# Kernel tuning notes

Measured on AMD Instinct MI355X. Metric: run time of the kernel, lower is better.

Reference implementation:

```python
import jax, jax.numpy as jnp
import numpy as np

N_NEAR = 16
BN_EPS = 1e-5


def fps(xyz, n_center):
    # farthest point sampling, deterministic start at index 0. xyz: [B,N,C]
    B, N, _ = xyz.shape
    dist0 = jnp.full((B, N), jnp.inf, dtype=xyz.dtype)
    far0 = jnp.zeros((B,), dtype=jnp.int32)

    def step(carry, _):
        dist, far = carry
        centroid = jnp.take_along_axis(xyz, far[:, None, None], axis=1)  # [B,1,C]
        d = jnp.sum((xyz - centroid) ** 2, axis=-1)                       # [B,N]
        dist = jnp.minimum(dist, d)
        nxt = jnp.argmax(dist, axis=-1).astype(jnp.int32)
        return (dist, nxt), far

    _, idxs = jax.lax.scan(step, (dist0, far0), None, length=n_center)
    return jnp.transpose(idxs)  # [B, n_center]


def knn(xyz, k):
    # k nearest neighbors (self included), xyz: [B,N,C] -> idx [B,N,k]
    sq = jnp.sum(xyz * xyz, axis=-1)
    d = sq[:, :, None] - 2.0 * jnp.einsum('bnc,bmc->bnm', xyz, xyz) + sq[:, None, :]
    _, idx = jax.lax.top_k(-d, k)
    return idx


def gather_points(x, idx):
    # x: [B,N,...], idx: [B,*dims] int -> [B,*dims,...]
    return jax.vmap(lambda xb, ib: xb[ib])(x, idx)


def conv_bn_relu(x, W, b, g, be):
    # x: [B,C,K,S]; 1x1 Conv2d + BatchNorm2d (training/batch stats) + ReLU
    y = jnp.einsum('oc,bcks->boks', W, x) + b[None, :, None, None]
    mean = jnp.mean(y, axis=(0, 2, 3), keepdims=True)
    var = jnp.mean((y - mean) ** 2, axis=(0, 2, 3), keepdims=True)  # biased var, as torch BN
    y = (y - mean) * jax.lax.rsqrt(var + BN_EPS)
    y = y * g[None, :, None, None] + be[None, :, None, None]
    return jax.nn.relu(y)


def setup_inputs() -> dict:
    key = jax.random.key(0)
    ks = jax.random.split(key, 8)
    B, N, EMB = 16, 2048, 64
    mlp = [64, 128, 256]
    in_ch = 2 + EMB
    inp = {
        'xy': jax.random.normal(ks[0], (B, 2, N), dtype=jnp.float32),
        'fea': jax.random.normal(ks[1], (B, EMB, N), dtype=jnp.float32),
    }
    last = in_ch
    for i, out in enumerate(mlp):
        inp[f'W{i+1}'] = 0.1 * jax.random.normal(ks[2 + i], (out, last), dtype=jnp.float32)
        inp[f'b{i+1}'] = jnp.zeros((out,), dtype=jnp.float32)
        inp[f'g{i+1}'] = jnp.ones((out,), dtype=jnp.float32)
        inp[f'be{i+1}'] = jnp.zeros((out,), dtype=jnp.float32)
        last = out
    return inp


def reference(xy, fea, W1, b1, g1, be1, W2, b2, g2, be2, W3, b3, g3, be3):
    B, _, N = xy.shape
    n_center = N // 2 + 1
    xyz = jnp.transpose(xy, (0, 2, 1))   # [B,N,2]
    f = jnp.transpose(fea, (0, 2, 1))    # [B,N,emb]

    fps_idx = fps(xyz, n_center)                      # [B,S]
    new_xyz = gather_points(xyz, fps_idx)             # [B,S,2]
    knn_idx = knn(xyz, N_NEAR)                        # [B,N,k]
    knn_of_fps = gather_points(knn_idx, fps_idx)      # [B,S,k]
    grouped_xyz = gather_points(xyz, knn_of_fps)      # [B,S,k,2]
    grouped_norm = grouped_xyz - new_xyz[:, :, None, :]
    grouped_f = gather_points(f, knn_of_fps)          # [B,S,k,emb]
    new_fea = jnp.concatenate([grouped_norm, grouped_f], axis=-1)  # [B,S,k,C]

    x = jnp.transpose(new_fea, (0, 3, 2, 1))          # [B,C,k,S]
    for (W, b, g, be) in ((W1, b1, g1, be1), (W2, b2, g2, be2), (W3, b3, g3, be3)):
        x = conv_bn_relu(x, W, b, g, be)
    out = jnp.max(x, axis=2)                          # [B,C_out,S]
    return jnp.transpose(new_xyz, (0, 2, 1)), out
```

## Files before the change

kernel.cpp:

```cpp
#include <hip/hip_runtime.h>
#include <math.h>

#define B_   16
#define N_   2048
#define S_   1025
#define K_   16
#define EMB_ 64
#define NF_  (B_ * S_ * K_)
#define NCH_ (NF_ / 64)
#define NBS_ (NCH_ * 4)
#define NBLK 256
#define PK_UNITS 513
#define KNN_ITEMS (129 * 16)

typedef float v2f __attribute__((ext_vector_type(2)));
typedef short bf16x8 __attribute__((ext_vector_type(8)));
typedef float f32x4 __attribute__((ext_vector_type(4)));

#define AL(p)    __hip_atomic_load((p), __ATOMIC_ACQUIRE, __HIP_MEMORY_SCOPE_AGENT)
#define ALR(p)   __hip_atomic_load((p), __ATOMIC_RELAXED, __HIP_MEMORY_SCOPE_AGENT)
#define ASR(p,v) __hip_atomic_store((p), (v), __ATOMIC_RELEASE, __HIP_MEMORY_SCOPE_AGENT)
#define AADD(p)  __hip_atomic_fetch_add((p), 1, __ATOMIC_ACQ_REL, __HIP_MEMORY_SCOPE_AGENT)

__device__ __forceinline__ unsigned short f2bf(float f) {
  unsigned u = __float_as_uint(f);
  u += 0x7fffu + ((u >> 16) & 1u);
  return (unsigned short)(u >> 16);
}
__device__ __forceinline__ float bfl(unsigned pk) { return __uint_as_float((pk & 0xffffu) << 16); }
__device__ __forceinline__ float bfh(unsigned pk) { return __uint_as_float(pk & 0xffff0000u); }

__device__ __forceinline__ float rowsum16(float v) {
#define RADD(CTRL) { int tm_ = __builtin_amdgcn_update_dpp(0, __float_as_int(v), (CTRL), 0xF, 0xF, true); \
                     v += __int_as_float(tm_); }
  RADD(0x111) RADD(0x112) RADD(0x114) RADD(0x118)
#undef RADD
  return v;
}

__global__ void diag_kernel(float* out, float v) {
  if (threadIdx.x == 0 && blockIdx.x == 0) out[0] = v;
}

__global__ __launch_bounds__(256, 1)
void phase0_kernel(const float* __restrict__ xy, const float* __restrict__ fea,
                   const float* __restrict__ W1,
                   const float* __restrict__ W2, const float* __restrict__ W3,
                   int* fps_idx, float* new_xyz, int* knn_sel,
                   unsigned* Pp, unsigned short* W2b, unsigned short* W3b,
                   float* out0, int* flags) {
  __shared__ float2 sh_lxy[N_];
  __shared__ double sh_lsq[N_];
  __shared__ float sh_pkA[4096];
  __shared__ float sh_pkB[4096];
  __shared__ int sh_unit;
  const int bid = blockIdx.x;
  const int tid = threadIdx.x;
  int* progress = flags + 8;

  if (bid < 16) {
    const int b = bid;
    const int lane = tid;
    const float* xb = xy + (size_t)b * 2 * N_;
    v2f pxp[16], pyp[16];
    float dist[32];
    if (lane < 64) {
      const float2* xb2 = (const float2*)xb;
      const float2* yb2 = (const float2*)(xb + N_);
#pragma unroll
      for (int q = 0; q < 16; ++q) {
        float2 x01 = xb2[lane * 16 + q];
        float2 y01 = yb2[lane * 16 + q];
        int p = lane * 32 + 2 * q;
        sh_lxy[p] = make_float2(x01.x, y01.x);
        sh_lxy[p + 1] = make_float2(x01.y, y01.y);
        pxp[q][0] = x01.x; pxp[q][1] = x01.y;
        pyp[q][0] = y01.x; pyp[q][1] = y01.y;
        dist[2 * q] = __builtin_inff();
        dist[2 * q + 1] = __builtin_inff();
      }
#pragma unroll
      for (int q = 0; q < 16; ++q) {
        asm volatile("" : "+v"(pxp[q]), "+v"(pyp[q]));
      }
    }
    __syncthreads();
    if (lane < 64) {
      int cur = 0;
      for (int t = 0; t < S_; ++t) {
        float2 c = sh_lxy[cur];
        if (lane == 0) {
          fps_idx[b * S_ + t] = cur;
          new_xyz[(b * S_ + t) * 2 + 0] = c.x;
          new_xyz[(b * S_ + t) * 2 + 1] = c.y;
          out0[b * 2 * S_ + t] = c.x;
          out0[b * 2 * S_ + S_ + t] = c.y;
        }
        const float ncx = -c.x, ncy = -c.y;
        v2f ncx2; ncx2[0] = ncx; ncx2[1] = ncx;
        v2f ncy2; ncy2[0] = ncy; ncy2[1] = ncy;
#pragma unroll
        for (int q = 0; q < 16; ++q) {
          v2f dx, dy, sx, sy, dd;
          asm("v_pk_add_f32 %0, %1, %2" : "=v"(dx) : "v"(pxp[q]), "v"(ncx2));
          asm("v_pk_add_f32 %0, %1, %2" : "=v"(dy) : "v"(pyp[q]), "v"(ncy2));
          asm("v_pk_mul_f32 %0, %1, %1" : "=v"(sx) : "v"(dx));
          asm("v_pk_mul_f32 %0, %1, %1" : "=v"(sy) : "v"(dy));
          asm("v_pk_add_f32 %0, %1, %2" : "=v"(dd) : "v"(sx), "v"(sy));
          dist[2 * q] = fminf(dist[2 * q], dd[0]);
          dist[2 * q + 1] = fminf(dist[2 * q + 1], dd[1]);
        }
        float m1[16], m2[8], m3[4], m4[2];
#pragma unroll
        for (int j = 0; j < 16; ++j) m1[j] = fmaxf(dist[2 * j], dist[2 * j + 1]);
#pragma unroll
        for (int j = 0; j < 8; ++j) m2[j] = fmaxf(m1[2 * j], m1[2 * j + 1]);
#pragma unroll
        for (int j = 0; j < 4; ++j) m3[j] = fmaxf(m2[2 * j], m2[2 * j + 1]);
        m4[0] = fmaxf(m3[0], m3[1]);
        m4[1] = fmaxf(m3[2], m3[3]);
        const float lmax = fmaxf(m4[0], m4[1]);
        int xr = __float_as_int(lmax);
#define DPP_MAX_STEP(CTRL)                                                        \
        {                                                                         \
          int tmp_ = __builtin_amdgcn_update_dpp(xr, xr, (CTRL), 0xF, 0xF, false);\
          xr = __float_as_int(fmaxf(__int_as_float(xr), __int_as_float(tmp_)));   \
        }
        DPP_MAX_STEP(0x111)
        DPP_MAX_STEP(0x112)
        DPP_MAX_STEP(0x114)
        DPP_MAX_STEP(0x118)
        DPP_MAX_STEP(0x142)
        DPP_MAX_STEP(0x143)
#undef DPP_MAX_STEP
        const float g = __int_as_float(__builtin_amdgcn_readlane(xr, 63));
        int n = (m4[0] == g) ? 0 : 1;
        float c3 = (n & 1) ? m3[2] : m3[0];
        n = 2 * n + ((c3 == g) ? 0 : 1);
        float lo2 = (n & 1) ? m2[2] : m2[0];
        float hi2 = (n & 1) ? m2[6] : m2[4];
        float c2 = (n & 2) ? hi2 : lo2;
        n = 2 * n + ((c2 == g) ? 0 : 1);
        float a0 = (n & 1) ? m1[2] : m1[0];
        float a1v = (n & 1) ? m1[6] : m1[4];
        float a2v = (n & 1) ? m1[10] : m1[8];
        float a3v = (n & 1) ? m1[14] : m1[12];
        float b0 = (n & 2) ? a1v : a0;
        float b1v = (n & 2) ? a3v : a2v;
        float c1 = (n & 4) ? b1v : b0;
        n = 2 * n + ((c1 == g) ? 0 : 1);
        float e0 = (n & 1) ? dist[2] : dist[0];
        float e1 = (n & 1) ? dist[6] : dist[4];
        float e2 = (n & 1) ? dist[10] : dist[8];
        float e3 = (n & 1) ? dist[14] : dist[12];
        float e4 = (n & 1) ? dist[18] : dist[16];
        float e5 = (n & 1) ? dist[22] : dist[20];
        float e6 = (n & 1) ? dist[26] : dist[24];
        float e7 = (n & 1) ? dist[30] : dist[28];
        float f0 = (n & 2) ? e1 : e0;
        float f1 = (n & 2) ? e3 : e2;
        float f2 = (n & 2) ? e5 : e4;
        float f3 = (n & 2) ? e7 : e6;
        float g0 = (n & 4) ? f1 : f0;
        float g1v = (n & 4) ? f3 : f2;
        float c0 = (n & 8) ? g1v : g0;
        const int lf = 2 * n + ((c0 == g) ? 0 : 1);
        unsigned long long mask = __ballot(lmax == g);
        int first = __ffsll(mask) - 1;
        cur = __builtin_amdgcn_readlane(lane * 32 + lf, first);
        if (lane == 0 && ((t & 31) == 31 || t == S_ - 1)) {
          ASR(&progress[b], t + 1);
        }
      }
    }
  } else {
    for (;;) {
      __syncthreads();
      if (tid == 0) sh_unit = AADD(&flags[2]);
      __syncthreads();
      int u = sh_unit;
      if (u >= PK_UNITS) break;
      if (u < 512) {
        const int b = u >> 5;
        const int pt0 = (u & 31) << 6;
#pragma unroll
        for (int p = 0; p < 16; ++p) {
          int idx = tid + 256 * p;
          int c = idx >> 6, e = idx & 63;
          sh_pkA[e * 64 + c] = W1[c * 66 + 2 + e];
          int r = (tid >> 6) + 4 * p, cc = tid & 63;
          sh_pkB[r * 64 + cc] = fea[((size_t)b * 64 + r) * N_ + pt0 + cc];
        }
        __syncthreads();
        const int tpt = tid & 15, tcq = tid >> 4;
        float acc[4][4];
#pragma unroll
        for (int i = 0; i < 4; ++i)
#pragma unroll
          for (int j = 0; j < 4; ++j) acc[i][j] = 0.f;
        for (int e = 0; e < 64; ++e) {
          float4 a4 = *reinterpret_cast<const float4*>(&sh_pkA[e * 64 + tcq * 4]);
          float4 b4 = *reinterpret_cast<const float4*>(&sh_pkB[e * 64 + tpt * 4]);
          const float av[4] = {a4.x, a4.y, a4.z, a4.w};
          const float bvv[4] = {b4.x, b4.y, b4.z, b4.w};
#pragma unroll
          for (int i = 0; i < 4; ++i)
#pragma unroll
            for (int j = 0; j < 4; ++j) acc[i][j] = fmaf(av[i], bvv[j], acc[i][j]);
        }
#pragma unroll
        for (int j = 0; j < 4; ++j) {
          int pt = tpt * 4 + j;
          unsigned lo = (unsigned)f2bf(acc[0][j]) | ((unsigned)f2bf(acc[1][j]) << 16);
          unsigned hi = (unsigned)f2bf(acc[2][j]) | ((unsigned)f2bf(acc[3][j]) << 16);
          unsigned* dst = &Pp[((size_t)(b * N_ + pt0 + pt)) * 32 + tcq * 2];
          dst[0] = lo;
          dst[1] = hi;
        }
      } else {
        for (int i = tid; i < 128 * 64; i += 256) W2b[i] = f2bf(W2[i]);
        for (int i = tid; i < 256 * 128; i += 256) W3b[i] = f2bf(W3[i]);
      }
    }
    for (;;) {
      __syncthreads();
      if (tid == 0) sh_unit = AADD(&flags[4]);
      __syncthreads();
      int it = sh_unit;
      if (it >= KNN_ITEMS) break;
      const int b = it & 15;
      const int s0 = (it >> 4) * 8;
      const int sHi = (s0 + 8 < S_) ? (s0 + 8) : S_;
      if (tid == 0) {
        while (AL(&progress[b]) < sHi) __builtin_amdgcn_s_sleep(8);
      }
      __syncthreads();
      const float* xb = xy + (size_t)b * 2 * N_;
      for (int p = tid; p < N_; p += 256) {
        float x = xb[p], y = xb[N_ + p];
        sh_lxy[p] = make_float2(x, y);
        sh_lsq[p] = (double)x * (double)x + (double)y * (double)y;
      }
      __syncthreads();
      const int s = s0 + (tid >> 5);
      const int oct = tid & 31;
      if (s < S_) {
        const int p0 = ALR((int*)&fps_idx[b * S_ + s]);
        float2 q = sh_lxy[p0];
        const double xn = (double)q.x, yn = (double)q.y;
        const double sqn = sh_lsq[p0];
        double d16[16];
        int i16[16];
#pragma unroll
        for (int j = 0; j < 16; ++j) { d16[j] = __builtin_inf(); i16[j] = 0x7fffffff; }
        const int mlo = oct * 64;
        for (int m0 = mlo; m0 < mlo + 64; m0 += 4) {
          double dd[4];
#pragma unroll
          for (int u2 = 0; u2 < 4; ++u2) {
            float2 p = sh_lxy[m0 + u2];
            double dot = (double)p.x * xn + (double)p.y * yn;
            dd[u2] = (sqn - 2.0 * dot) + sh_lsq[m0 + u2];
          }
#pragma unroll
          for (int u2 = 0; u2 < 4; ++u2) {
            if (dd[u2] < d16[15]) {
              double d = dd[u2];
              int mi = m0 + u2;
#pragma unroll
              for (int j = 15; j >= 1; --j) {
                bool shift = d < d16[j - 1];
                bool ins = d < d16[j];
                d16[j] = shift ? d16[j - 1] : (ins ? d : d16[j]);
                i16[j] = shift ? i16[j - 1] : (ins ? mi : i16[j]);
              }
              if (d < d16[0]) { d16[0] = d; i16[0] = mi; }
            }
          }
        }
#pragma unroll
        for (int w = 1; w <= 16; w <<= 1) {
          double nd[16]; int ni[16];
#pragma unroll
          for (int i = 0; i < 16; ++i) {
            double rd = __shfl_xor(d16[15 - i], w, 64);
            int ri = __shfl_xor(i16[15 - i], w, 64);
            bool takeR = (rd < d16[i]) || (rd == d16[i] && ri < i16[i]);
            nd[i] = takeR ? rd : d16[i];
            ni[i] = takeR ? ri : i16[i];
          }
#pragma unroll
          for (int i = 0; i < 16; ++i) { d16[i] = nd[i]; i16[i] = ni[i]; }
          if (w < 16) {
#pragma unroll
            for (int dstg = 8; dstg >= 1; dstg >>= 1) {
#pragma unroll
              for (int i = 0; i < 16; ++i) {
                if ((i & dstg) == 0) {
                  int a = i, c = i + dstg;
                  bool sw = (d16[a] > d16[c]) || (d16[a] == d16[c] && i16[a] > i16[c]);
                  double tlo = sw ? d16[c] : d16[a];
                  double thi = sw ? d16[a] : d16[c];
                  int ulo = sw ? i16[c] : i16[a];
                  int uhi = sw ? i16[a] : i16[c];
                  d16[a] = tlo; d16[c] = thi; i16[a] = ulo; i16[c] = uhi;
                }
              }
            }
          }
        }
        if (oct == 0) {
          int* dst = knn_sel + ((size_t)b * S_ + s) * K_;
#pragma unroll
          for (int j = 0; j < 16; ++j) dst[j] = i16[j];
        }
      }
    }
  }
}

__global__ __launch_bounds__(256) void yk1_kernel(const float* __restrict__ xy,
                                                  const int* __restrict__ knn_sel,
                                                  const float* __restrict__ new_xyz,
                                                  const unsigned* __restrict__ Pp,
                                                  const float* __restrict__ W1,
                                                  const float* __restrict__ b1,
                                                  unsigned* __restrict__ Y1p) {
  __shared__ float w0s[64], w1s[64], bbs[64];
  const int t = threadIdx.x;
  if (t < 64) { w0s[t] = W1[t * 66 + 0]; w1s[t] = W1[t * 66 + 1]; bbs[t] = b1[t]; }
  __syncthreads();
  const int n = blockIdx.x * 256 + t;
  const int bs = n >> 4;
  const int b = bs / S_;
  const int nbr = knn_sel[n];
  const float dx = xy[(size_t)b * 2 * N_ + nbr] - new_xyz[bs * 2 + 0];
  const float dy = xy[(size_t)b * 2 * N_ + N_ + nbr] - new_xyz[bs * 2 + 1];
  const unsigned* prow = &Pp[((size_t)(b * N_ + nbr)) * 32];
#pragma unroll 8
  for (int j = 0; j < 32; ++j) {
    unsigned pj = prow[j];
    int c = 2 * j;
    float v0 = bfl(pj) + w0s[c] * dx + w1s[c] * dy + bbs[c];
    float v1 = bfh(pj) + w0s[c + 1] * dx + w1s[c + 1] * dy + bbs[c + 1];
    Y1p[(size_t)j * NF_ + n] = (unsigned)f2bf(v0) | ((unsigned)f2bf(v1) << 16);
  }
}

__global__ __launch_bounds__(256) void rowstats_kernel(const unsigned* __restrict__ Y1p,
                                                       float* __restrict__ parts) {
  const int j = blockIdx.x & 31;
  const int seg = blockIdx.x >> 5;
  const int SEG = NF_ / 8;
  const unsigned* p = Y1p + (size_t)j * NF_ + (size_t)seg * SEG;
  double s0 = 0, q0 = 0, s1 = 0, q1 = 0;
  for (int i = threadIdx.x; i < SEG; i += 256) {
    unsigned pk = p[i];
    double a = (double)bfl(pk), b = (double)bfh(pk);
    s0 += a; q0 = fma(a, a, q0);
    s1 += b; q1 = fma(b, b, q1);
  }
  __shared__ double sh[4][256];
  sh[0][threadIdx.x] = s0; sh[1][threadIdx.x] = q0;
  sh[2][threadIdx.x] = s1; sh[3][threadIdx.x] = q1;
  __syncthreads();
  for (int o = 128; o > 0; o >>= 1) {
    if (threadIdx.x < o) {
#pragma unroll
      for (int u = 0; u < 4; ++u) sh[u][threadIdx.x] += sh[u][threadIdx.x + o];
    }
    __syncthreads();
  }
  if (threadIdx.x == 0) {
    float* dst = parts + (size_t)(j * 8 + seg) * 4;
    dst[0] = (float)sh[0][0];
    dst[1] = (float)sh[2][0];
    dst[2] = (float)sh[1][0];
    dst[3] = (float)sh[3][0];
  }
}

__global__ void redabsch1_kernel(const float* __restrict__ parts,
                                 const float* __restrict__ g, const float* __restrict__ be,
                                 float* __restrict__ A, float* __restrict__ D) {
  int m = threadIdx.x;
  if (m >= 64) return;
  int j = m >> 1, par = m & 1;
  double a = 0.0, b = 0.0;
  for (int seg = 0; seg < 8; ++seg) {
    const float* src = parts + (size_t)(j * 8 + seg) * 4;
    a += (double)src[par];
    b += (double)src[2 + par];
  }
  double mu = a * (1.0 / NF_);
  double var = b * (1.0 / NF_) - mu * mu;
  double aa = (double)g[m] / sqrt(var + 1e-5);
  A[m] = (float)aa;
  D[m] = (float)((double)be[m] - aa * mu);
}

__global__ void redabsch_kernel(const float* __restrict__ parts, int P, int M,
                                const float* __restrict__ g, const float* __restrict__ be,
                                float* __restrict__ A, float* __restrict__ D) {
  int m = threadIdx.x;
  if (m >= M) return;
  double a = 0.0, b = 0.0;
  for (int p = 0; p < P; ++p) {
    a += (double)parts[(size_t)p * 2 * M + m];
    b += (double)parts[(size_t)p * 2 * M + M + m];
  }
  double mu = a * (1.0 / NF_);
  double var = b * (1.0 / NF_) - mu * mu;
  double aa = (double)g[m] / sqrt(var + 1e-5);
  A[m] = (float)aa;
  D[m] = (float)((double)be[m] - aa * mu);
}

__device__ __forceinline__ void stage_x1(const unsigned* Y1p, const float* ab1, char* x1c,
                                         size_t n0, int w, int L) {
#pragma unroll
  for (int e = 0; e < 8; ++e) {
    int k0 = 2 * (w + 4 * e);
    unsigned pkv = Y1p[(size_t)(k0 >> 1) * NF_ + n0 + L];
    float v0 = fmaxf(fmaf(bfl(pkv), ab1[k0], ab1[64 + k0]), 0.f);
    float v1 = fmaxf(fmaf(bfh(pkv), ab1[k0 + 1], ab1[64 + k0 + 1]), 0.f);
    unsigned pk = (unsigned)f2bf(v0) | ((unsigned)f2bf(v1) << 16);
    *reinterpret_cast<unsigned*>(&x1c[L * 128 + ((2 * k0) ^ ((L & 7) << 4))]) = pk;
  }
}

__global__ __launch_bounds__(256) void passA_mfma_kernel(
    const unsigned* __restrict__ Y1p, const unsigned short* __restrict__ W2b,
    const float* __restrict__ A1v, const float* __restrict__ Bc1v,
    float* __restrict__ parts) {
  __shared__ float ab1[128];
  __shared__ __align__(16) unsigned short x1b[64 * 64];
  const int t = threadIdx.x;
  const int w = t >> 6, L = t & 63;
  if (t < 128) ab1[t] = (t < 64) ? A1v[t] : Bc1v[t - 64];
  bf16x8 w2f[2][2];
#pragma unroll
  for (int rb = 0; rb < 2; ++rb)
#pragma unroll
    for (int ks = 0; ks < 2; ++ks) {
      int row = (2 * w + rb) * 16 + (L & 15);
      int koff = ks * 32 + (L >> 4) * 8;
      w2f[rb][ks] = *reinterpret_cast<const bf16x8*>(&W2b[row * 64 + koff]);
    }
  float vs[2][4], vq[2][4];
#pragma unroll
  for (int rb = 0; rb < 2; ++rb)
#pragma unroll
    for (int r = 0; r < 4; ++r) { vs[rb][r] = 0.f; vq[rb][r] = 0.f; }
  char* x1c = reinterpret_cast<char*>(x1b);
  for (int ch = blockIdx.x; ch < NCH_; ch += 512) {
    const size_t n0 = (size_t)ch * 64;
    __syncthreads();
    stage_x1(Y1p, ab1, x1c, n0, w, L);
    __syncthreads();
#pragma unroll
    for (int rb = 0; rb < 2; ++rb) {
      f32x4 acc2[4];
#pragma unroll
      for (int cb = 0; cb < 4; ++cb) acc2[cb][0] = acc2[cb][1] = acc2[cb][2] = acc2[cb][3] = 0.f;
#pragma unroll
      for (int ks = 0; ks < 2; ++ks)
#pragma unroll
        for (int cb = 0; cb < 4; ++cb) {
          int n = cb * 16 + (L & 15);
          int koff = ks * 32 + (L >> 4) * 8;
          bf16x8 bfr = *reinterpret_cast<const bf16x8*>(&x1c[n * 128 + ((2 * koff) ^ ((n & 7) << 4))]);
          acc2[cb] = __builtin_amdgcn_mfma_f32_16x16x32_bf16(w2f[rb][ks], bfr, acc2[cb], 0, 0, 0);
        }
#pragma unroll
      for (int cb = 0; cb < 4; ++cb)
#pragma unroll
        for (int r = 0; r < 4; ++r) {
          float y = acc2[cb][r];
          vs[rb][r] += y;
          vq[rb][r] = fmaf(y, y, vq[rb][r]);
        }
    }
  }
#pragma unroll
  for (int rb = 0; rb < 2; ++rb)
#pragma unroll
    for (int r = 0; r < 4; ++r) {
      float s = rowsum16(vs[rb][r]);
      float q = rowsum16(vq[rb][r]);
      if ((L & 15) == 15) {
        int row = (2 * w + rb) * 16 + (L >> 4) * 4 + r;
        parts[(size_t)blockIdx.x * 256 + row] = s;
        parts[(size_t)blockIdx.x * 256 + 128 + row] = q;
      }
    }
}

__global__ __launch_bounds__(256) void passB_mfma_kernel(
    const unsigned* __restrict__ Y1p,
    const unsigned short* __restrict__ W2b, const unsigned short* __restrict__ W3b,
    const float* __restrict__ A1v, const float* __restrict__ Bc1v,
    const float* __restrict__ A2v, const float* __restrict__ D2v,
    float* __restrict__ parts, unsigned* __restrict__ M3) {
  __shared__ float ab1[128];
  __shared__ __align__(16) unsigned short x1b[64 * 64];
  __shared__ __align__(16) unsigned short x2b[64 * 128];
  const int t = threadIdx.x;
  const int w = t >> 6, L = t & 63;
  if (t < 128) ab1[t] = (t < 64) ? A1v[t] : Bc1v[t - 64];
  bf16x8 w3f[4][4];
#pragma unroll
  for (int rb = 0; rb < 4; ++rb)
#pragma unroll
    for (int ks = 0; ks < 4; ++ks) {
      int row = (4 * w + rb) * 16 + (L & 15);
      int koff = ks * 32 + (L >> 4) * 8;
      w3f[rb][ks] = *reinterpret_cast<const bf16x8*>(&W3b[row * 128 + koff]);
    }
  bf16x8 w2f[2][2];
#pragma unroll
  for (int rb = 0; rb < 2; ++rb)
#pragma unroll
    for (int ks = 0; ks < 2; ++ks) {
      int row = (2 * w + rb) * 16 + (L & 15);
      int koff = ks * 32 + (L >> 4) * 8;
      w2f[rb][ks] = *reinterpret_cast<const bf16x8*>(&W2b[row * 64 + koff]);
    }
  float vs[4][4], vq[4][4];
#pragma unroll
  for (int rb = 0; rb < 4; ++rb)
#pragma unroll
    for (int r = 0; r < 4; ++r) { vs[rb][r] = 0.f; vq[rb][r] = 0.f; }
  char* x1c = reinterpret_cast<char*>(x1b);
  char* x2c = reinterpret_cast<char*>(x2b);
  for (int ch = blockIdx.x; ch < NCH_; ch += 256) {
    const size_t n0 = (size_t)ch * 64;
    __syncthreads();
    stage_x1(Y1p, ab1, x1c, n0, w, L);
    __syncthreads();
#pragma unroll
    for (int rb = 0; rb < 2; ++rb) {
      f32x4 acc2[4];
#pragma unroll
      for (int cb = 0; cb < 4; ++cb) acc2[cb][0] = acc2[cb][1] = acc2[cb][2] = acc2[cb][3] = 0.f;
#pragma unroll
      for (int ks = 0; ks < 2; ++ks)
#pragma unroll
        for (int cb = 0; cb < 4; ++cb) {
          int n = cb * 16 + (L & 15);
          int koff = ks * 32 + (L >> 4) * 8;
          bf16x8 bfr = *reinterpret_cast<const bf16x8*>(&x1c[n * 128 + ((2 * koff) ^ ((n & 7) << 4))]);
          acc2[cb] = __builtin_amdgcn_mfma_f32_16x16x32_bf16(w2f[rb][ks], bfr, acc2[cb], 0, 0, 0);
        }
#pragma unroll
      for (int cb = 0; cb < 4; ++cb) {
        int n = cb * 16 + (L & 15);
        int kbase = (2 * w + rb) * 16 + (L >> 4) * 4;
#pragma unroll
        for (int rp = 0; rp < 2; ++rp) {
          int r0 = 2 * rp;
          float a0 = A2v[kbase + r0], d0 = D2v[kbase + r0];
          float a1 = A2v[kbase + r0 + 1], d1 = D2v[kbase + r0 + 1];
          float v0 = fmaxf(fmaf(acc2[cb][r0], a0, d0), 0.f);
          float v1 = fmaxf(fmaf(acc2[cb][r0 + 1], a1, d1), 0.f);
          unsigned pk = (unsigned)f2bf(v0) | ((unsigned)f2bf(v1) << 16);
          int k0 = kbase + r0;
          *reinterpret_cast<unsigned*>(&x2c[n * 256 + ((2 * k0) ^ ((n & 7) << 4))]) = pk;
        }
      }
    }
    __syncthreads();
    bf16x8 b3[4][4];
#pragma unroll
    for (int cb = 0; cb < 4; ++cb)
#pragma unroll
      for (int ks = 0; ks < 4; ++ks) {
        int n = cb * 16 + (L & 15);
        int koff = ks * 32 + (L >> 4) * 8;
        b3[cb][ks] = *reinterpret_cast<const bf16x8*>(&x2c[n * 256 + ((2 * koff) ^ ((n & 7) << 4))]);
      }
#pragma unroll
    for (int rb = 0; rb < 4; ++rb) {
      f32x4 acc3[4];
#pragma unroll
      for (int cb = 0; cb < 4; ++cb) acc3[cb][0] = acc3[cb][1] = acc3[cb][2] = acc3[cb][3] = 0.f;
#pragma unroll
      for (int ks = 0; ks < 4; ++ks)
#pragma unroll
        for (int cb = 0; cb < 4; ++cb)
          acc3[cb] = __builtin_amdgcn_mfma_f32_16x16x32_bf16(w3f[rb][ks], b3[cb][ks], acc3[cb], 0, 0, 0);
#pragma unroll
      for (int cb = 0; cb < 4; ++cb)
#pragma unroll
        for (int r = 0; r < 4; ++r) {
          float y = acc3[cb][r];
          vs[rb][r] += y;
          vq[rb][r] = fmaf(y, y, vq[rb][r]);
        }
      {
        int rowbase = (4 * w + rb) * 16 + (L >> 4) * 4;
#pragma unroll
        for (int cb = 0; cb < 4; ++cb) {
#pragma unroll
          for (int r = 0; r < 4; ++r) {
            float v = acc3[cb][r];
            int xi = __float_as_int(v), xm = __float_as_int(v);
#define RMAX(CTRL) { int tm_ = __builtin_amdgcn_update_dpp(xi, xi, (CTRL), 0xF, 0xF, false); \
                     xi = __float_as_int(fmaxf(__int_as_float(xi), __int_as_float(tm_))); }
#define RMIN(CTRL) { int tm_ = __builtin_amdgcn_update_dpp(xm, xm, (CTRL), 0xF, 0xF, false); \
                     xm = __float_as_int(fminf(__int_as_float(xm), __int_as_float(tm_))); }
            RMAX(0x111) RMAX(0x112) RMAX(0x114) RMAX(0x118)
            RMIN(0x111) RMIN(0x112) RMIN(0x114) RMIN(0x118)
#undef RMAX
#undef RMIN
            if ((L & 15) == 15) {
              int row = rowbase + r;
              int bs = ch * 4 + cb;
              M3[(size_t)row * NBS_ + bs] =
                  (unsigned)f2bf(__int_as_float(xi)) | ((unsigned)f2bf(__int_as_float(xm)) << 16);
            }
          }
        }
      }
    }
  }
#pragma unroll
  for (int rb = 0; rb < 4; ++rb)
#pragma unroll
    for (int r = 0; r < 4; ++r) {
      float s = rowsum16(vs[rb][r]);
      float q = rowsum16(vq[rb][r]);
      if ((L & 15) == 15) {
        int row = (4 * w + rb) * 16 + (L >> 4) * 4 + r;
        parts[(size_t)blockIdx.x * 512 + row] = s;
        parts[(size_t)blockIdx.x * 512 + 256 + row] = q;
      }
    }
}

__global__ __launch_bounds__(256) void final_small_kernel(
    const unsigned* __restrict__ M3, const float* __restrict__ A3,
    const float* __restrict__ D3, float* __restrict__ out1) {
  int gid = blockIdx.x * 256 + threadIdx.x;
  int row = gid / NBS_, bs = gid - row * NBS_;
  unsigned pk = M3[gid];
  float vmax = bfl(pk);
  float vmin = bfh(pk);
  float a = A3[row];
  float v = (a >= 0.f) ? vmax : vmin;
  int b = bs / S_, s = bs - b * S_;
  out1[((size_t)(b * 256 + row)) * S_ + s] = fmaxf(fmaf(v, a, D3[row]), 0.f);
}

extern "C" void kernel_launch(void* const* d_in, const int* in_sizes, int n_in,
                              void* d_out, int out_size, void* d_ws, size_t ws_size,
                              hipStream_t stream) {
  const float* xy  = (const float*)d_in[0];
  const float* fea = (const float*)d_in[1];
  const float* W1  = (const float*)d_in[2];
  const float* b1  = (const float*)d_in[3];
  const float* g1  = (const float*)d_in[4];
  const float* be1 = (const float*)d_in[5];
  const float* W2  = (const float*)d_in[6];
  const float* g2  = (const float*)d_in[8];
  const float* be2 = (const float*)d_in[9];
  const float* W3  = (const float*)d_in[10];
  const float* g3  = (const float*)d_in[12];
  const float* be3 = (const float*)d_in[13];
  float* out = (float*)d_out;
  float* out1 = out + B_ * 2 * S_;

  char* w = (char*)d_ws;
  size_t off = 0;
  auto take = [&](size_t bytes) -> void* {
    void* p = w + off;
    off += (bytes + 255) & ~(size_t)255;
    return p;
  };
  int*      flags   = (int*)take(256);
  int*      fps_idx = (int*)take((size_t)B_ * S_ * 4);
  float*    new_xyz = (float*)take((size_t)B_ * S_ * 2 * 4);
  int*      knn_sel = (int*)take((size_t)NF_ * 4);
  unsigned* Pp      = (unsigned*)take((size_t)B_ * N_ * 32 * 4);
  unsigned* Y1p     = (unsigned*)take((size_t)32 * NF_ * 4);
  float*    parts1  = (float*)take((size_t)256 * 4 * 4);
  float*    A1      = (float*)take(64 * 4);
  float*    Bc1     = (float*)take(64 * 4);
  float*    partsA  = (float*)take((size_t)512 * 256 * 4);
  float*    A2      = (float*)take(128 * 4);
  float*    D2      = (float*)take(128 * 4);
  float*    partsB  = (float*)take((size_t)256 * 512 * 4);
  float*    A3      = (float*)take(256 * 4);
  float*    D3      = (float*)take(256 * 4);
  unsigned short* W2b = (unsigned short*)take((size_t)128 * 64 * 2);
  unsigned short* W3b = (unsigned short*)take((size_t)256 * 128 * 2);
  unsigned* M3      = (unsigned*)take((size_t)256 * NBS_ * 4);

  if (off > ws_size) {
    diag_kernel<<<1, 64, 0, stream>>>(out, (float)(ws_size >> 20));
    return;
  }

  hipMemsetAsync(flags, 0, 256, stream);
  phase0_kernel<<<NBLK, 256, 0, stream>>>(xy, fea, W1, W2, W3, fps_idx, new_xyz,
                                          knn_sel, Pp, W2b, W3b, out, flags);
  yk1_kernel<<<NF_ / 256, 256, 0, stream>>>(xy, knn_sel, new_xyz, Pp, W1, b1, Y1p);

  rowstats_kernel<<<256, 256, 0, stream>>>(Y1p, parts1);
  redabsch1_kernel<<<1, 64, 0, stream>>>(parts1, g1, be1, A1, Bc1);

  passA_mfma_kernel<<<512, 256, 0, stream>>>(Y1p, W2b, A1, Bc1, partsA);
  redabsch_kernel<<<1, 128, 0, stream>>>(partsA, 512, 128, g2, be2, A2, D2);

  passB_mfma_kernel<<<256, 256, 0, stream>>>(Y1p, W2b, W3b, A1, Bc1, A2, D2, partsB, M3);
  redabsch_kernel<<<1, 256, 0, stream>>>(partsB, 256, 256, g3, be3, A3, D3);

  final_small_kernel<<<(256 * NBS_) / 256, 256, 0, stream>>>(M3, A3, D3, out1);
}
```

Before: 1.234 ms.

## Statically assign KNN work per block and pad per-batch progress flags

Replaces the atomic work-queue for KNN items with a static assignment: each of the 240 worker blocks is bound to one batch, loads that batch's point cloud into shared memory once, then strides over its chunks of centers. Per-batch FPS progress counters are moved to separate 64-byte-spaced slots to avoid false sharing, and the fps_idx read becomes an acquire load. This removes the repeated shared-memory reload and the atomic fetch per item, at the cost of losing dynamic load balancing if some batches' FPS runs behind.

```diff
diff --git a/kernel.cpp b/kernel.cpp
--- a/kernel.cpp
+++ b/kernel.cpp
@@ -11,14 +11,12 @@
 #define NBS_ (NCH_ * 4)
 #define NBLK 256
 #define PK_UNITS 513
-#define KNN_ITEMS (129 * 16)
 
 typedef float v2f __attribute__((ext_vector_type(2)));
 typedef short bf16x8 __attribute__((ext_vector_type(8)));
 typedef float f32x4 __attribute__((ext_vector_type(4)));
 
 #define AL(p)    __hip_atomic_load((p), __ATOMIC_ACQUIRE, __HIP_MEMORY_SCOPE_AGENT)
-#define ALR(p)   __hip_atomic_load((p), __ATOMIC_RELAXED, __HIP_MEMORY_SCOPE_AGENT)
 #define ASR(p,v) __hip_atomic_store((p), (v), __ATOMIC_RELEASE, __HIP_MEMORY_SCOPE_AGENT)
 #define AADD(p)  __hip_atomic_fetch_add((p), 1, __ATOMIC_ACQ_REL, __HIP_MEMORY_SCOPE_AGENT)
 
@@ -56,7 +54,7 @@
   __shared__ int sh_unit;
   const int bid = blockIdx.x;
   const int tid = threadIdx.x;
-  int* progress = flags + 8;
+#define PROG(bb) (flags + 16 + 16 * (bb))
 
   if (bid < 16) {
     const int b = bid;
@@ -169,7 +167,7 @@
         int first = __ffsll(mask) - 1;
         cur = __builtin_amdgcn_readlane(lane * 32 + lf, first);
         if (lane == 0 && ((t & 31) == 31 || t == S_ - 1)) {
-          ASR(&progress[b], t + 1);
+          ASR(PROG(b), t + 1);
         }
       }
     }
@@ -222,37 +220,35 @@
         for (int i = tid; i < 256 * 128; i += 256) W3b[i] = f2bf(W3[i]);
       }
     }
-    for (;;) {
-      __syncthreads();
-      if (tid == 0) sh_unit = AADD(&flags[4]);
-      __syncthreads();
-      int it = sh_unit;
-      if (it >= KNN_ITEMS) break;
-      const int b = it & 15;
-      const int s0 = (it >> 4) * 8;
+    const int wk = bid - 16;
+    const int b = wk & 15;
+    const int j0 = wk >> 4;
+    const float* xb = xy + (size_t)b * 2 * N_;
+    __syncthreads();
+    for (int p = tid; p < N_; p += 256) {
+      float x = xb[p], y = xb[N_ + p];
+      sh_lxy[p] = make_float2(x, y);
+      sh_lsq[p] = (double)x * (double)x + (double)y * (double)y;
+    }
+    __syncthreads();
+    for (int j = j0; j < 129; j += 15) {
+      const int s0 = j * 8;
       const int sHi = (s0 + 8 < S_) ? (s0 + 8) : S_;
       if (tid == 0) {
-        while (AL(&progress[b]) < sHi) __builtin_amdgcn_s_sleep(8);
-      }
-      __syncthreads();
-      const float* xb = xy + (size_t)b * 2 * N_;
-      for (int p = tid; p < N_; p += 256) {
-        float x = xb[p], y = xb[N_ + p];
-        sh_lxy[p] = make_float2(x, y);
-        sh_lsq[p] = (double)x * (double)x + (double)y * (double)y;
+        while (AL(PROG(b)) < sHi) __builtin_amdgcn_s_sleep(8);
       }
       __syncthreads();
       const int s = s0 + (tid >> 5);
       const int oct = tid & 31;
       if (s < S_) {
-        const int p0 = ALR((int*)&fps_idx[b * S_ + s]);
+        const int p0 = AL((int*)&fps_idx[b * S_ + s]);
         float2 q = sh_lxy[p0];
         const double xn = (double)q.x, yn = (double)q.y;
         const double sqn = sh_lsq[p0];
         double d16[16];
         int i16[16];
 #pragma unroll
-        for (int j = 0; j < 16; ++j) { d16[j] = __builtin_inf(); i16[j] = 0x7fffffff; }
+        for (int jj = 0; jj < 16; ++jj) { d16[jj] = __builtin_inf(); i16[jj] = 0x7fffffff; }
         const int mlo = oct * 64;
         for (int m0 = mlo; m0 < mlo + 64; m0 += 4) {
           double dd[4];
@@ -268,11 +264,11 @@
               double d = dd[u2];
               int mi = m0 + u2;
 #pragma unroll
-              for (int j = 15; j >= 1; --j) {
-                bool shift = d < d16[j - 1];
-                bool ins = d < d16[j];
-                d16[j] = shift ? d16[j - 1] : (ins ? d : d16[j]);
-                i16[j] = shift ? i16[j - 1] : (ins ? mi : i16[j]);
+              for (int jj = 15; jj >= 1; --jj) {
+                bool shift = d < d16[jj - 1];
+                bool ins = d < d16[jj];
+                d16[jj] = shift ? d16[jj - 1] : (ins ? d : d16[jj]);
+                i16[jj] = shift ? i16[jj - 1] : (ins ? mi : i16[jj]);
               }
               if (d < d16[0]) { d16[0] = d; i16[0] = mi; }
             }
@@ -312,11 +308,12 @@
         if (oct == 0) {
           int* dst = knn_sel + ((size_t)b * S_ + s) * K_;
 #pragma unroll
-          for (int j = 0; j < 16; ++j) dst[j] = i16[j];
-        }
-      }
-    }
-  }
+          for (int jj = 0; jj < 16; ++jj) dst[jj] = i16[jj];
+        }
+      }
+    }
+  }
+#undef PROG
 }
 
 __global__ __launch_bounds__(256) void yk1_kernel(const float* __restrict__ xy,
@@ -677,7 +674,7 @@
     off += (bytes + 255) & ~(size_t)255;
     return p;
   };
-  int*      flags   = (int*)take(256);
+  int*      flags   = (int*)take(2048);
   int*      fps_idx = (int*)take((size_t)B_ * S_ * 4);
   float*    new_xyz = (float*)take((size_t)B_ * S_ * 2 * 4);
   int*      knn_sel = (int*)take((size_t)NF_ * 4);
@@ -701,7 +698,7 @@
     return;
   }
 
-  hipMemsetAsync(flags, 0, 256, stream);
+  hipMemsetAsync(flags, 0, 2048, stream);
   phase0_kernel<<<NBLK, 256, 0, stream>>>(xy, fea, W1, W2, W3, fps_idx, new_xyz,
                                           knn_sel, Pp, W2b, W3b, out, flags);
   yk1_kernel<<<NF_ / 256, 256, 0, stream>>>(xy, knn_sel, new_xyz, Pp, W1, b1, Y1p);
```

Result: no change. 1.225 ms (-0.7%).
